# Optimization experiments

Hardware: AMD Instinct MI355X
Metric: run time of the kernel (lower is better)

The kernel has to match this reference:

```python
import jax, jax.numpy as jnp
import numpy as np

B, L, C, R = 2, 1024, 64, 32
RV, DQK, H, NSINK = 32, 64, 8, 4


def setup_inputs() -> dict:
    key = jax.random.key(0)
    ks = jax.random.split(key, 10)
    s_in = 1.0 / np.sqrt(C * R)
    s_r = 1.0 / np.sqrt(R)
    s_rv = 1.0 / np.sqrt(RV)
    return {
        "x": jax.random.normal(ks[0], (B, L, C, R), jnp.float32),
        "Wq": jax.random.normal(ks[1], (C * R, H * DQK), jnp.float32) * s_in,
        "bq": jax.random.normal(ks[2], (H * DQK,), jnp.float32) * s_in,
        "Wk": jax.random.normal(ks[3], (C * R, DQK), jnp.float32) * s_in,
        "bk": jax.random.normal(ks[4], (DQK,), jnp.float32) * s_in,
        "Wv": jax.random.normal(ks[5], (C, R, RV), jnp.float32) * s_r,
        "bv": jax.random.normal(ks[6], (C, RV), jnp.float32) * s_r,
        "Wo": jax.random.normal(ks[7], (C, RV, R), jnp.float32) * s_rv,
        "bo": jax.random.normal(ks[8], (C, R), jnp.float32) * s_rv,
        "sink_q": jax.random.normal(ks[9], (H, NSINK, DQK), jnp.float32),
    }


def reference(x, Wq, bq, Wk, bk, Wv, bv, Wo, bo, sink_q):
    b, l, c, r = x.shape
    h, d_qk = H, DQK
    scale = 1.0 / np.sqrt(d_qk)

    x_flat = x.reshape(b, l, c * r)
    q = (x_flat @ Wq + bq).reshape(b, l, h, d_qk)          # (B,L,H,D)
    k = x_flat @ Wk + bk                                    # (B,L,D) shared MQA key

    # fp32 softmax over time, as in the original
    logits = (jnp.einsum('blhd,bsd->bhls', q, k).astype(jnp.float32) * scale)
    attn = jax.nn.softmax(logits, axis=-1).astype(x.dtype)  # (B,H,L,S)

    # per-channel value projection (B,L,C,RV)
    v = jnp.einsum('blcr,cro->blco', x, Wv) + bv

    # AV with extra channel axis, fused with head-mean (same math as
    # einsum('bhls,bscv->bhlcv').mean(1))
    y = jnp.einsum('bhls,bscv->blcv', attn, v) / h          # (B,L,C,RV)

    # sink-query branch: learned queries attend over time, mean over (H, S)
    logits_s = (jnp.einsum('hsd,bld->bhsl', sink_q, k).astype(jnp.float32) * scale)
    attn_s = jax.nn.softmax(logits_s, axis=-1).astype(x.dtype)  # (B,H,S,L)
    y_sink = jnp.einsum('bhsl,blcv->bcv', attn_s, v) / (h * NSINK)
    y = y + y_sink[:, None]                                 # broadcast over L

    # per-channel output projection + residual
    y = jnp.einsum('blcv,cvr->blcr', y, Wo) + bo
    return x + y
```

## Files before the change

### kernel.cpp

```cpp
#include <hip/hip_runtime.h>
#include <hip/hip_bf16.h>
#include <math.h>


typedef __attribute__((ext_vector_type(8))) short short8;
typedef __attribute__((ext_vector_type(4))) short short4v;
typedef __attribute__((ext_vector_type(4))) float float4v;

__device__ __forceinline__ short f2b(float f) {
    __hip_bfloat16 h = __float2bfloat16(f);
    return __builtin_bit_cast(short, h);
}
__device__ __forceinline__ float b2f(short s) {
    unsigned u = ((unsigned)(unsigned short)s) << 16;
    return __builtin_bit_cast(float, u);
}

__global__ __launch_bounds__(256) void convert_x_kernel(
    const float* __restrict__ src, short* __restrict__ dst, int n4)
{
    int id = blockIdx.x * 256 + threadIdx.x;
    if (id >= n4) return;
    float4 v = reinterpret_cast<const float4*>(src)[id];
    short4v o;
    o[0] = f2b(v.x); o[1] = f2b(v.y); o[2] = f2b(v.z); o[3] = f2b(v.w);
    reinterpret_cast<short4v*>(dst)[id] = o;
}

__global__ __launch_bounds__(256) void convert_w_kernel(
    const float* __restrict__ Wq, const float* __restrict__ Wk,
    short* __restrict__ Wt)
{
    const int n0 = blockIdx.x * 64;
    const int k0 = blockIdx.y * 64;
    const int tid = threadIdx.x;
    __shared__ float ts[64][65];
    for (int i = tid; i < 4096; i += 256) {
        int kk = i >> 6, nn = i & 63;
        int n = n0 + nn, k = k0 + kk;
        float v = (n < 512) ? Wq[(long)k * 512 + n] : Wk[(long)k * 64 + (n - 512)];
        ts[kk][nn] = v;
    }
    __syncthreads();
    for (int i = tid; i < 4096; i += 256) {
        int nn = i >> 6, kk = i & 63;
        Wt[(long)(n0 + nn) * 2048 + k0 + kk] = f2b(ts[kk][nn]);
    }
}

__global__ __launch_bounds__(256) void bias_init_kernel(
    const float* __restrict__ bq, const float* __restrict__ bk,
    float* __restrict__ qk)
{
    const int row = blockIdx.x;
    for (int n = threadIdx.x; n < 576; n += 256)
        qk[(long)row * 576 + n] = (n < 512) ? bq[n] : bk[n - 512];
}

__global__ __launch_bounds__(256) void qkproj_kernel(
    const short* __restrict__ xb, const short* __restrict__ Wt,
    float* __restrict__ qk)
{
    __shared__ short As[64][72];
    __shared__ short Bs[64][72];

    const int tid = threadIdx.x;
    const int wave = tid >> 6;
    const int lane = tid & 63;
    const int wm = wave >> 1, wn = wave & 1;
    const int m15 = lane & 15;
    const int quad = lane >> 4;
    const int row0 = blockIdx.y * 64;
    const int col0 = blockIdx.x * 64;
    const int kbase = blockIdx.z * 1024;

    float4v acc[2][2];
    #pragma unroll
    for (int i = 0; i < 2; ++i)
        #pragma unroll
        for (int j = 0; j < 2; ++j)
            #pragma unroll
            for (int r = 0; r < 4; ++r) acc[i][j][r] = 0.f;

    for (int kt = 0; kt < 16; ++kt) {
        int k0 = kbase + kt * 64;
        #pragma unroll
        for (int p = 0; p < 2; ++p) {
            int i = tid + p * 256;
            int m = i >> 3, kq = i & 7;
            *reinterpret_cast<short8*>(&As[m][kq * 8]) =
                *reinterpret_cast<const short8*>(&xb[(long)(row0 + m) * 2048 + k0 + kq * 8]);
        }
        #pragma unroll
        for (int p = 0; p < 2; ++p) {
            int i = tid + p * 256;
            int n = i >> 3, kq = i & 7;
            *reinterpret_cast<short8*>(&Bs[n][kq * 8]) =
                *reinterpret_cast<const short8*>(&Wt[(long)(col0 + n) * 2048 + k0 + kq * 8]);
        }
        __syncthreads();
        #pragma unroll
        for (int ks = 0; ks < 2; ++ks) {
            short8 a[2], b[2];
            #pragma unroll
            for (int t = 0; t < 2; ++t) {
                a[t] = *reinterpret_cast<const short8*>(&As[wm * 32 + t * 16 + m15][ks * 32 + quad * 8]);
                b[t] = *reinterpret_cast<const short8*>(&Bs[wn * 32 + t * 16 + m15][ks * 32 + quad * 8]);
            }
            #pragma unroll
            for (int ti = 0; ti < 2; ++ti)
                #pragma unroll
                for (int tj = 0; tj < 2; ++tj)
                    acc[ti][tj] = __builtin_amdgcn_mfma_f32_16x16x32_bf16(
                        a[ti], b[tj], acc[ti][tj], 0, 0, 0);
        }
        __syncthreads();
    }

    #pragma unroll
    for (int ti = 0; ti < 2; ++ti)
        #pragma unroll
        for (int r = 0; r < 4; ++r) {
            int row = row0 + wm * 32 + ti * 16 + quad * 4 + r;
            #pragma unroll
            for (int tj = 0; tj < 2; ++tj) {
                int col = col0 + wn * 32 + tj * 16 + m15;
                atomicAdd(&qk[(long)row * 576 + col], acc[ti][tj][r]);
            }
        }
}

__global__ __launch_bounds__(256) void convert_qk_kernel(
    const float* __restrict__ qk, short* __restrict__ qkb)
{
    int id = blockIdx.x * 256 + threadIdx.x;
    float4 v = reinterpret_cast<const float4*>(qk)[id];
    short4v o;
    o[0] = f2b(v.x); o[1] = f2b(v.y); o[2] = f2b(v.z); o[3] = f2b(v.w);
    reinterpret_cast<short4v*>(qkb)[id] = o;
}

__global__ __launch_bounds__(256) void qk_s_kernel(
    const short* __restrict__ qkb, short* __restrict__ S)
{
    const int s0 = blockIdx.x * 64;
    const int l0 = blockIdx.y * 64;
    const int b = blockIdx.z;
    const int tid = threadIdx.x;
    short* Sz = S + ((long)b << 23);

    __shared__ short Qs[64][520];
    __shared__ short Ks[64][72];

    #pragma unroll
    for (int p = 0; p < 16; ++p) {
        int i = tid + p * 256;
        int row = i >> 6, d8 = i & 63;
        *reinterpret_cast<short8*>(&Qs[row][d8 * 8]) =
            *reinterpret_cast<const short8*>(&qkb[(long)((b << 10) + l0 + row) * 576 + d8 * 8]);
    }
    #pragma unroll
    for (int p = 0; p < 2; ++p) {
        int i = tid + p * 256;
        int row = i >> 3, d8 = i & 7;
        *reinterpret_cast<short8*>(&Ks[row][d8 * 8]) =
            *reinterpret_cast<const short8*>(&qkb[(long)((b << 10) + s0 + row) * 576 + 512 + d8 * 8]);
    }
    __syncthreads();

    const int wave = tid >> 6;
    const int lane = tid & 63;
    const int wm = wave >> 1, wn = wave & 1;
    const int m15 = lane & 15;
    const int quad = lane >> 4;

    for (int h = 0; h < 8; ++h) {
        float4v acc[2][2];
        #pragma unroll
        for (int i = 0; i < 2; ++i)
            #pragma unroll
            for (int j = 0; j < 2; ++j)
                #pragma unroll
                for (int r = 0; r < 4; ++r) acc[i][j][r] = 0.f;

        #pragma unroll
        for (int ks = 0; ks < 2; ++ks) {
            short8 a[2], bfr[2];
            #pragma unroll
            for (int t = 0; t < 2; ++t) {
                a[t]   = *reinterpret_cast<const short8*>(
                    &Qs[wm * 32 + t * 16 + m15][h * 64 + ks * 32 + quad * 8]);
                bfr[t] = *reinterpret_cast<const short8*>(
                    &Ks[wn * 32 + t * 16 + m15][ks * 32 + quad * 8]);
            }
            #pragma unroll
            for (int ti = 0; ti < 2; ++ti)
                #pragma unroll
                for (int tj = 0; tj < 2; ++tj)
                    acc[ti][tj] = __builtin_amdgcn_mfma_f32_16x16x32_bf16(
                        a[ti], bfr[tj], acc[ti][tj], 0, 0, 0);
        }

        #pragma unroll
        for (int ti = 0; ti < 2; ++ti)
            #pragma unroll
            for (int r = 0; r < 4; ++r) {
                int l = l0 + wm * 32 + ti * 16 + quad * 4 + r;
                #pragma unroll
                for (int tj = 0; tj < 2; ++tj) {
                    int s = s0 + wn * 32 + tj * 16 + m15;
                    Sz[((long)h << 20) + (l << 10) + s] = f2b(acc[ti][tj][r] * 0.125f);
                }
            }
    }
}

__global__ __launch_bounds__(256) void softmax_avg_kernel(
    const short* __restrict__ S, short* __restrict__ P)
{
    const int l = blockIdx.x;
    const int b = blockIdx.y;
    const int tid = threadIdx.x;
    const int h = tid >> 5, j = tid & 31;
    const short* Sz = S + ((long)b << 23);

    __shared__ float es[8][1032];
    __shared__ float invd[8];

    const short* row = &Sz[((long)h << 20) + (l << 10)];
    float vals[32];
    float pm = -1e30f;
    #pragma unroll
    for (int i = 0; i < 32; ++i) {
        float f = b2f(row[i * 32 + j]);
        vals[i] = f;
        pm = fmaxf(pm, f);
    }
    #pragma unroll
    for (int off = 16; off > 0; off >>= 1) pm = fmaxf(pm, __shfl_down(pm, off, 32));
    pm = __shfl(pm, 0, 32);

    float ps = 0.f;
    #pragma unroll
    for (int i = 0; i < 32; ++i) {
        float e = __expf(vals[i] - pm);
        vals[i] = e;
        ps += e;
    }
    #pragma unroll
    for (int off = 16; off > 0; off >>= 1) ps += __shfl_down(ps, off, 32);
    if (j == 0) invd[h] = 1.f / (8.f * ps);
    __syncthreads();

    const float w = invd[h];
    #pragma unroll
    for (int i = 0; i < 32; ++i) es[h][i * 32 + j] = vals[i] * w;
    __syncthreads();

    for (int s = tid; s < 1024; s += 256) {
        float p = 0.f;
        #pragma unroll
        for (int hh = 0; hh < 8; ++hh) p += es[hh][s];
        P[((long)b << 20) + (l << 10) + s] = f2b(p);
    }
}

__global__ __launch_bounds__(256) void vproj_kernel(
    const float* __restrict__ x, const float* __restrict__ Wv,
    const float* __restrict__ bv, short* __restrict__ vt)
{
    const int c = blockIdx.x;
    const int chunk = blockIdx.y;
    const int b = chunk >> 4;
    const int l0 = (chunk & 15) * 64;
    const int tid = threadIdx.x;
    __shared__ float Wc[32][33];
    __shared__ float xs[64][33];
    for (int i = tid; i < 1024; i += 256)
        Wc[i >> 5][i & 31] = Wv[(c * 32 + (i >> 5)) * 32 + (i & 31)];
    for (int i = tid; i < 2048; i += 256) {
        int s = i >> 5, r = i & 31;
        xs[s][r] = x[((long)(b << 10) + l0 + s) * 2048 + c * 32 + r];
    }
    __syncthreads();
    const int s = tid & 63;
    const int og = tid >> 6;
    #pragma unroll
    for (int oi = 0; oi < 8; ++oi) {
        int o = og * 8 + oi;
        float acc = bv[c * 32 + o];
        #pragma unroll
        for (int r = 0; r < 32; ++r) acc += xs[s][r] * Wc[r][o];
        vt[(long)b * (2048 * 1024) + (long)(c * 32 + o) * 1024 + l0 + s] = f2b(acc);
    }
}

__global__ __launch_bounds__(256) void sink_kernel(
    const float* __restrict__ sink_q, const short* __restrict__ qkb,
    float* __restrict__ Psink)
{
    const int z = blockIdx.x;
    const int b = z >> 5;
    const int idx = z & 31;
    const int tid = threadIdx.x;

    __shared__ float sq[64];
    __shared__ float lgl[1024];
    __shared__ float red[4];
    __shared__ float mxs, invs;

    if (tid < 64) sq[tid] = sink_q[idx * 64 + tid];
    __syncthreads();

    float lmax = -1e30f;
    for (int l = tid; l < 1024; l += 256) {
        const short* kp = &qkb[(long)((b << 10) + l) * 576 + 512];
        float acc = 0.f;
        #pragma unroll
        for (int d8 = 0; d8 < 8; ++d8) {
            short8 kv = *reinterpret_cast<const short8*>(&kp[d8 * 8]);
            #pragma unroll
            for (int j = 0; j < 8; ++j) acc += b2f(kv[j]) * sq[d8 * 8 + j];
        }
        acc *= 0.125f;
        lgl[l] = acc;
        lmax = fmaxf(lmax, acc);
    }
    #pragma unroll
    for (int off = 32; off > 0; off >>= 1) lmax = fmaxf(lmax, __shfl_down(lmax, off, 64));
    if ((tid & 63) == 0) red[tid >> 6] = lmax;
    __syncthreads();
    if (tid == 0) mxs = fmaxf(fmaxf(red[0], red[1]), fmaxf(red[2], red[3]));
    __syncthreads();

    const float m = mxs;
    float psum = 0.f;
    for (int l = tid; l < 1024; l += 256) {
        float e = __expf(lgl[l] - m);
        lgl[l] = e;
        psum += e;
    }
    #pragma unroll
    for (int off = 32; off > 0; off >>= 1) psum += __shfl_down(psum, off, 64);
    if ((tid & 63) == 0) red[tid >> 6] = psum;
    __syncthreads();
    if (tid == 0) invs = 1.f / (red[0] + red[1] + red[2] + red[3]);
    __syncthreads();

    const float wgt = invs * (1.f / 32.f);
    for (int l = tid; l < 1024; l += 256)
        atomicAdd(&Psink[(b << 10) + l], lgl[l] * wgt);
}

__global__ __launch_bounds__(256) void sinky_kernel(
    const float* __restrict__ Psink, const short* __restrict__ vt,
    float* __restrict__ Ysink)
{
    const int b = blockIdx.y;
    const int tid = threadIdx.x;
    __shared__ float ps[1024];
    {
        float4 v = reinterpret_cast<const float4*>(&Psink[b << 10])[tid];
        *reinterpret_cast<float4*>(&ps[tid * 4]) = v;
    }
    __syncthreads();
    const int wave = tid >> 6;
    const int lane = tid & 63;
    const int co = blockIdx.x * 4 + wave;
    const short* vp = &vt[((long)b * 2048 + co) * 1024];
    float acc = 0.f;
    #pragma unroll
    for (int t = 0; t < 16; ++t) {
        int l = t * 64 + lane;
        acc += ps[l] * b2f(vp[l]);
    }
    #pragma unroll
    for (int off = 32; off > 0; off >>= 1) acc += __shfl_down(acc, off, 64);
    if (lane == 0) Ysink[(b << 11) + co] = acc;
}

__global__ __launch_bounds__(256) void y_fused_kernel(
    const short* __restrict__ P, const short* __restrict__ vt,
    const float* __restrict__ Ysink, const float* __restrict__ Wo,
    const float* __restrict__ bo, const float* __restrict__ x,
    float* __restrict__ out)
{
    __shared__ short As[64][72];
    __shared__ short Bs[64][72];

    const int tid = threadIdx.x;
    const int b = blockIdx.z;
    const int col0 = blockIdx.x * 64;
    const int row0 = blockIdx.y * 64;
    const short* Pz = P + ((long)b << 20);
    const short* Vz = vt + ((long)b * 2048 * 1024);

    const int wave = tid >> 6;
    const int lane = tid & 63;
    const int wm = wave >> 1, wn = wave & 1;
    const int m15 = lane & 15;
    const int quad = lane >> 4;

    float4v acc[2][2];
    #pragma unroll
    for (int i = 0; i < 2; ++i)
        #pragma unroll
        for (int j = 0; j < 2; ++j)
            #pragma unroll
            for (int r = 0; r < 4; ++r) acc[i][j][r] = 0.f;

    for (int kt = 0; kt < 16; ++kt) {
        int k0 = kt * 64;
        #pragma unroll
        for (int p = 0; p < 2; ++p) {
            int i = tid + p * 256;
            int m = i >> 3, kq = i & 7;
            *reinterpret_cast<short8*>(&As[m][kq * 8]) =
                *reinterpret_cast<const short8*>(&Pz[(long)(row0 + m) * 1024 + k0 + kq * 8]);
        }
        #pragma unroll
        for (int p = 0; p < 2; ++p) {
            int i = tid + p * 256;
            int n = i >> 3, kq = i & 7;
            *reinterpret_cast<short8*>(&Bs[n][kq * 8]) =
                *reinterpret_cast<const short8*>(&Vz[(long)(col0 + n) * 1024 + k0 + kq * 8]);
        }
        __syncthreads();
        #pragma unroll
        for (int ks = 0; ks < 2; ++ks) {
            short8 a[2], bb[2];
            #pragma unroll
            for (int t = 0; t < 2; ++t) {
                a[t]  = *reinterpret_cast<const short8*>(&As[wm * 32 + t * 16 + m15][ks * 32 + quad * 8]);
                bb[t] = *reinterpret_cast<const short8*>(&Bs[wn * 32 + t * 16 + m15][ks * 32 + quad * 8]);
            }
            #pragma unroll
            for (int ti = 0; ti < 2; ++ti)
                #pragma unroll
                for (int tj = 0; tj < 2; ++tj)
                    acc[ti][tj] = __builtin_amdgcn_mfma_f32_16x16x32_bf16(
                        a[ti], bb[tj], acc[ti][tj], 0, 0, 0);
        }
        __syncthreads();
    }

    float ysv[2];
    #pragma unroll
    for (int tj = 0; tj < 2; ++tj)
        ysv[tj] = Ysink[(b << 11) + col0 + wn * 32 + tj * 16 + m15];

    #pragma unroll
    for (int ti = 0; ti < 2; ++ti)
        #pragma unroll
        for (int r = 0; r < 4; ++r) {
            int row = wm * 32 + ti * 16 + quad * 4 + r;
            #pragma unroll
            for (int tj = 0; tj < 2; ++tj) {
                int col = wn * 32 + tj * 16 + m15;
                As[row][col] = f2b(acc[ti][tj][r] + ysv[tj]);
            }
        }
    const int c0 = col0 >> 5;
    for (int i = tid; i < 4096; i += 256) {
        int n = i >> 6, k = i & 63;
        short v = 0;
        if ((n >> 5) == (k >> 5))
            v = f2b(Wo[((long)(c0 + (n >> 5)) * 32 + (k & 31)) * 32 + (n & 31)]);
        Bs[n][k] = v;
    }
    __syncthreads();

    float4v acc2[2][2];
    #pragma unroll
    for (int i = 0; i < 2; ++i)
        #pragma unroll
        for (int j = 0; j < 2; ++j)
            #pragma unroll
            for (int r = 0; r < 4; ++r) acc2[i][j][r] = 0.f;

    #pragma unroll
    for (int ks = 0; ks < 2; ++ks) {
        short8 a[2], bb[2];
        #pragma unroll
        for (int t = 0; t < 2; ++t) {
            a[t]  = *reinterpret_cast<const short8*>(&As[wm * 32 + t * 16 + m15][ks * 32 + quad * 8]);
            bb[t] = *reinterpret_cast<const short8*>(&Bs[wn * 32 + t * 16 + m15][ks * 32 + quad * 8]);
        }
        #pragma unroll
        for (int ti = 0; ti < 2; ++ti)
            #pragma unroll
            for (int tj = 0; tj < 2; ++tj)
                acc2[ti][tj] = __builtin_amdgcn_mfma_f32_16x16x32_bf16(
                    a[ti], bb[tj], acc2[ti][tj], 0, 0, 0);
    }

    float bov[2];
    #pragma unroll
    for (int tj = 0; tj < 2; ++tj)
        bov[tj] = bo[col0 + wn * 32 + tj * 16 + m15];

    #pragma unroll
    for (int ti = 0; ti < 2; ++ti)
        #pragma unroll
        for (int r = 0; r < 4; ++r) {
            int row = (b << 10) + row0 + wm * 32 + ti * 16 + quad * 4 + r;
            #pragma unroll
            for (int tj = 0; tj < 2; ++tj) {
                int col = col0 + wn * 32 + tj * 16 + m15;
                long oi = (long)row * 2048 + col;
                out[oi] = x[oi] + bov[tj] + acc2[ti][tj][r];
            }
        }
}

extern "C" void kernel_launch(void* const* d_in, const int* in_sizes, int n_in,
                              void* d_out, int out_size, void* d_ws, size_t ws_size,
                              hipStream_t stream)
{
    const float* x  = (const float*)d_in[0];
    const float* Wq = (const float*)d_in[1];
    const float* bq = (const float*)d_in[2];
    const float* Wk = (const float*)d_in[3];
    const float* bk = (const float*)d_in[4];
    const float* Wv = (const float*)d_in[5];
    const float* bv = (const float*)d_in[6];
    const float* Wo = (const float*)d_in[7];
    const float* bo = (const float*)d_in[8];
    const float* sq = (const float*)d_in[9];
    float* out = (float*)d_out;

    float* ws = (float*)d_ws;
    float* qk     = ws;
    short* qkb    = (short*)(ws + 1179648);
    short* P      = (short*)(ws + 1769472);
    float* Psink  = ws + 2818048;
    short* vt     = (short*)(ws + 2820096);
    float* Ysink  = ws + 4917248;
    float* region = ws + 4921344;
    short* xb     = (short*)region;
    short* Wt     = (short*)(region + 2097152);
    short* Sb     = (short*)region;

    dim3 blk(256);

    convert_x_kernel<<<dim3(1024 * 1024 / 256), blk, 0, stream>>>(x, xb, 1048576);
    convert_w_kernel<<<dim3(9, 32), blk, 0, stream>>>(Wq, Wk, Wt);
    bias_init_kernel<<<dim3(2048), blk, 0, stream>>>(bq, bk, qk);
    qkproj_kernel<<<dim3(9, 32, 2), blk, 0, stream>>>(xb, Wt, qk);
    convert_qk_kernel<<<dim3(1152), blk, 0, stream>>>(qk, qkb);
    vproj_kernel<<<dim3(64, 32), blk, 0, stream>>>(x, Wv, bv, vt);
    qk_s_kernel<<<dim3(16, 16, 2), blk, 0, stream>>>(qkb, Sb);
    softmax_avg_kernel<<<dim3(1024, 2), blk, 0, stream>>>(Sb, P);
    hipMemsetAsync(Psink, 0, 2048 * sizeof(float), stream);
    sink_kernel<<<dim3(64), blk, 0, stream>>>(sq, qkb, Psink);
    sinky_kernel<<<dim3(512, 2), blk, 0, stream>>>(Psink, vt, Ysink);
    y_fused_kernel<<<dim3(32, 16, 2), blk, 0, stream>>>(
        P, vt, Ysink, Wo, bo, x, out);
}
```

Measured before the change: 207.7 us.

## Fuse x conversion into vproj, replace split-K atomics with partial buffers, enlarge y tile

The bf16 conversion of x now happens inside the value-projection kernel, which already reads x, so the separate conversion pass and its extra read of x are gone. The split-K QK projection writes two partial buffers with plain stores instead of atomics into a bias-initialised buffer. The bf16 convert kernel then sums the two partials and adds the bias, which removes the bias-init kernel and the atomic traffic. The fused AV/output-projection kernel moves to 128-row tiles, halving the grid and reusing each loaded V tile across more rows, at the cost of more registers and shared memory per block.

```diff
diff --git a/kernel.cpp b/kernel.cpp
--- a/kernel.cpp
+++ b/kernel.cpp
@@ -14,17 +14,6 @@
 __device__ __forceinline__ float b2f(short s) {
     unsigned u = ((unsigned)(unsigned short)s) << 16;
     return __builtin_bit_cast(float, u);
-}
-
-__global__ __launch_bounds__(256) void convert_x_kernel(
-    const float* __restrict__ src, short* __restrict__ dst, int n4)
-{
-    int id = blockIdx.x * 256 + threadIdx.x;
-    if (id >= n4) return;
-    float4 v = reinterpret_cast<const float4*>(src)[id];
-    short4v o;
-    o[0] = f2b(v.x); o[1] = f2b(v.y); o[2] = f2b(v.z); o[3] = f2b(v.w);
-    reinterpret_cast<short4v*>(dst)[id] = o;
 }
 
 __global__ __launch_bounds__(256) void convert_w_kernel(
@@ -48,18 +37,43 @@
     }
 }
 
-__global__ __launch_bounds__(256) void bias_init_kernel(
-    const float* __restrict__ bq, const float* __restrict__ bk,
-    float* __restrict__ qk)
-{
-    const int row = blockIdx.x;
-    for (int n = threadIdx.x; n < 576; n += 256)
-        qk[(long)row * 576 + n] = (n < 512) ? bq[n] : bk[n - 512];
+__global__ __launch_bounds__(256) void vproj_kernel(
+    const float* __restrict__ x, const float* __restrict__ Wv,
+    const float* __restrict__ bv, short* __restrict__ vt,
+    short* __restrict__ xb)
+{
+    const int c = blockIdx.x;
+    const int chunk = blockIdx.y;
+    const int b = chunk >> 4;
+    const int l0 = (chunk & 15) * 64;
+    const int tid = threadIdx.x;
+    __shared__ float Wc[32][33];
+    __shared__ float xs[64][33];
+    for (int i = tid; i < 1024; i += 256)
+        Wc[i >> 5][i & 31] = Wv[(c * 32 + (i >> 5)) * 32 + (i & 31)];
+    for (int i = tid; i < 2048; i += 256) {
+        int s = i >> 5, r = i & 31;
+        long gi = ((long)(b << 10) + l0 + s) * 2048 + c * 32 + r;
+        float v = x[gi];
+        xs[s][r] = v;
+        xb[gi] = f2b(v);
+    }
+    __syncthreads();
+    const int s = tid & 63;
+    const int og = tid >> 6;
+    #pragma unroll
+    for (int oi = 0; oi < 8; ++oi) {
+        int o = og * 8 + oi;
+        float acc = bv[c * 32 + o];
+        #pragma unroll
+        for (int r = 0; r < 32; ++r) acc += xs[s][r] * Wc[r][o];
+        vt[(long)b * (2048 * 1024) + (long)(c * 32 + o) * 1024 + l0 + s] = f2b(acc);
+    }
 }
 
 __global__ __launch_bounds__(256) void qkproj_kernel(
     const short* __restrict__ xb, const short* __restrict__ Wt,
-    float* __restrict__ qk)
+    float* __restrict__ qkpart)
 {
     __shared__ short As[64][72];
     __shared__ short Bs[64][72];
@@ -73,6 +87,7 @@
     const int row0 = blockIdx.y * 64;
     const int col0 = blockIdx.x * 64;
     const int kbase = blockIdx.z * 1024;
+    float* outz = qkpart + (long)blockIdx.z * 1179648;
 
     float4v acc[2][2];
     #pragma unroll
@@ -125,18 +140,27 @@
             #pragma unroll
             for (int tj = 0; tj < 2; ++tj) {
                 int col = col0 + wn * 32 + tj * 16 + m15;
-                atomicAdd(&qk[(long)row * 576 + col], acc[ti][tj][r]);
+                outz[(long)row * 576 + col] = acc[ti][tj][r];
             }
         }
 }
 
 __global__ __launch_bounds__(256) void convert_qk_kernel(
-    const float* __restrict__ qk, short* __restrict__ qkb)
+    const float* __restrict__ qkpart, const float* __restrict__ bq,
+    const float* __restrict__ bk, short* __restrict__ qkb)
 {
     int id = blockIdx.x * 256 + threadIdx.x;
-    float4 v = reinterpret_cast<const float4*>(qk)[id];
+    float4 a = reinterpret_cast<const float4*>(qkpart)[id];
+    float4 b = reinterpret_cast<const float4*>(qkpart + 1179648)[id];
+    int col4 = (id % 144) * 4;
+    float4 bias = (col4 < 512)
+        ? *reinterpret_cast<const float4*>(&bq[col4])
+        : *reinterpret_cast<const float4*>(&bk[col4 - 512]);
     short4v o;
-    o[0] = f2b(v.x); o[1] = f2b(v.y); o[2] = f2b(v.z); o[3] = f2b(v.w);
+    o[0] = f2b(a.x + b.x + bias.x);
+    o[1] = f2b(a.y + b.y + bias.y);
+    o[2] = f2b(a.z + b.z + bias.z);
+    o[3] = f2b(a.w + b.w + bias.w);
     reinterpret_cast<short4v*>(qkb)[id] = o;
 }
 
@@ -265,36 +289,6 @@
     }
 }
 
-__global__ __launch_bounds__(256) void vproj_kernel(
-    const float* __restrict__ x, const float* __restrict__ Wv,
-    const float* __restrict__ bv, short* __restrict__ vt)
-{
-    const int c = blockIdx.x;
-    const int chunk = blockIdx.y;
-    const int b = chunk >> 4;
-    const int l0 = (chunk & 15) * 64;
-    const int tid = threadIdx.x;
-    __shared__ float Wc[32][33];
-    __shared__ float xs[64][33];
-    for (int i = tid; i < 1024; i += 256)
-        Wc[i >> 5][i & 31] = Wv[(c * 32 + (i >> 5)) * 32 + (i & 31)];
-    for (int i = tid; i < 2048; i += 256) {
-        int s = i >> 5, r = i & 31;
-        xs[s][r] = x[((long)(b << 10) + l0 + s) * 2048 + c * 32 + r];
-    }
-    __syncthreads();
-    const int s = tid & 63;
-    const int og = tid >> 6;
-    #pragma unroll
-    for (int oi = 0; oi < 8; ++oi) {
-        int o = og * 8 + oi;
-        float acc = bv[c * 32 + o];
-        #pragma unroll
-        for (int r = 0; r < 32; ++r) acc += xs[s][r] * Wc[r][o];
-        vt[(long)b * (2048 * 1024) + (long)(c * 32 + o) * 1024 + l0 + s] = f2b(acc);
-    }
-}
-
 __global__ __launch_bounds__(256) void sink_kernel(
     const float* __restrict__ sink_q, const short* __restrict__ qkb,
     float* __restrict__ Psink)
@@ -385,13 +379,13 @@
     const float* __restrict__ bo, const float* __restrict__ x,
     float* __restrict__ out)
 {
-    __shared__ short As[64][72];
+    __shared__ short As[128][72];
     __shared__ short Bs[64][72];
 
     const int tid = threadIdx.x;
     const int b = blockIdx.z;
     const int col0 = blockIdx.x * 64;
-    const int row0 = blockIdx.y * 64;
+    const int row0 = blockIdx.y * 128;
     const short* Pz = P + ((long)b << 20);
     const short* Vz = vt + ((long)b * 2048 * 1024);
 
@@ -401,9 +395,9 @@
     const int m15 = lane & 15;
     const int quad = lane >> 4;
 
-    float4v acc[2][2];
-    #pragma unroll
-    for (int i = 0; i < 2; ++i)
+    float4v acc[4][2];
+    #pragma unroll
+    for (int i = 0; i < 4; ++i)
         #pragma unroll
         for (int j = 0; j < 2; ++j)
             #pragma unroll
@@ -412,7 +406,7 @@
     for (int kt = 0; kt < 16; ++kt) {
         int k0 = kt * 64;
         #pragma unroll
-        for (int p = 0; p < 2; ++p) {
+        for (int p = 0; p < 4; ++p) {
             int i = tid + p * 256;
             int m = i >> 3, kq = i & 7;
             *reinterpret_cast<short8*>(&As[m][kq * 8]) =
@@ -428,14 +422,15 @@
         __syncthreads();
         #pragma unroll
         for (int ks = 0; ks < 2; ++ks) {
-            short8 a[2], bb[2];
-            #pragma unroll
-            for (int t = 0; t < 2; ++t) {
-                a[t]  = *reinterpret_cast<const short8*>(&As[wm * 32 + t * 16 + m15][ks * 32 + quad * 8]);
+            short8 a[4], bb[2];
+            #pragma unroll
+            for (int t = 0; t < 4; ++t)
+                a[t] = *reinterpret_cast<const short8*>(&As[wm * 64 + t * 16 + m15][ks * 32 + quad * 8]);
+            #pragma unroll
+            for (int t = 0; t < 2; ++t)
                 bb[t] = *reinterpret_cast<const short8*>(&Bs[wn * 32 + t * 16 + m15][ks * 32 + quad * 8]);
-            }
-            #pragma unroll
-            for (int ti = 0; ti < 2; ++ti)
+            #pragma unroll
+            for (int ti = 0; ti < 4; ++ti)
                 #pragma unroll
                 for (int tj = 0; tj < 2; ++tj)
                     acc[ti][tj] = __builtin_amdgcn_mfma_f32_16x16x32_bf16(
@@ -450,10 +445,10 @@
         ysv[tj] = Ysink[(b << 11) + col0 + wn * 32 + tj * 16 + m15];
 
     #pragma unroll
-    for (int ti = 0; ti < 2; ++ti)
+    for (int ti = 0; ti < 4; ++ti)
         #pragma unroll
         for (int r = 0; r < 4; ++r) {
-            int row = wm * 32 + ti * 16 + quad * 4 + r;
+            int row = wm * 64 + ti * 16 + quad * 4 + r;
             #pragma unroll
             for (int tj = 0; tj < 2; ++tj) {
                 int col = wn * 32 + tj * 16 + m15;
@@ -470,9 +465,9 @@
     }
     __syncthreads();
 
-    float4v acc2[2][2];
-    #pragma unroll
-    for (int i = 0; i < 2; ++i)
+    float4v acc2[4][2];
+    #pragma unroll
+    for (int i = 0; i < 4; ++i)
         #pragma unroll
         for (int j = 0; j < 2; ++j)
             #pragma unroll
@@ -480,14 +475,15 @@
 
     #pragma unroll
     for (int ks = 0; ks < 2; ++ks) {
-        short8 a[2], bb[2];
-        #pragma unroll
-        for (int t = 0; t < 2; ++t) {
-            a[t]  = *reinterpret_cast<const short8*>(&As[wm * 32 + t * 16 + m15][ks * 32 + quad * 8]);
+        short8 a[4], bb[2];
+        #pragma unroll
+        for (int t = 0; t < 4; ++t)
+            a[t] = *reinterpret_cast<const short8*>(&As[wm * 64 + t * 16 + m15][ks * 32 + quad * 8]);
+        #pragma unroll
+        for (int t = 0; t < 2; ++t)
             bb[t] = *reinterpret_cast<const short8*>(&Bs[wn * 32 + t * 16 + m15][ks * 32 + quad * 8]);
-        }
-        #pragma unroll
-        for (int ti = 0; ti < 2; ++ti)
+        #pragma unroll
+        for (int ti = 0; ti < 4; ++ti)
             #pragma unroll
             for (int tj = 0; tj < 2; ++tj)
                 acc2[ti][tj] = __builtin_amdgcn_mfma_f32_16x16x32_bf16(
@@ -500,10 +496,10 @@
         bov[tj] = bo[col0 + wn * 32 + tj * 16 + m15];
 
     #pragma unroll
-    for (int ti = 0; ti < 2; ++ti)
+    for (int ti = 0; ti < 4; ++ti)
         #pragma unroll
         for (int r = 0; r < 4; ++r) {
-            int row = (b << 10) + row0 + wm * 32 + ti * 16 + quad * 4 + r;
+            int row = (b << 10) + row0 + wm * 64 + ti * 16 + quad * 4 + r;
             #pragma unroll
             for (int tj = 0; tj < 2; ++tj) {
                 int col = col0 + wn * 32 + tj * 16 + m15;
@@ -530,30 +526,28 @@
     float* out = (float*)d_out;
 
     float* ws = (float*)d_ws;
-    float* qk     = ws;
-    short* qkb    = (short*)(ws + 1179648);
-    short* P      = (short*)(ws + 1769472);
-    float* Psink  = ws + 2818048;
-    short* vt     = (short*)(ws + 2820096);
-    float* Ysink  = ws + 4917248;
-    float* region = ws + 4921344;
+    float* qkpart = ws;
+    short* qkb    = (short*)(ws + 2359296);
+    short* P      = (short*)(ws + 2949120);
+    float* Psink  = ws + 3997696;
+    short* vt     = (short*)(ws + 3999744);
+    float* Ysink  = ws + 6096896;
+    float* region = ws + 6100992;
     short* xb     = (short*)region;
     short* Wt     = (short*)(region + 2097152);
     short* Sb     = (short*)region;
 
     dim3 blk(256);
 
-    convert_x_kernel<<<dim3(1024 * 1024 / 256), blk, 0, stream>>>(x, xb, 1048576);
     convert_w_kernel<<<dim3(9, 32), blk, 0, stream>>>(Wq, Wk, Wt);
-    bias_init_kernel<<<dim3(2048), blk, 0, stream>>>(bq, bk, qk);
-    qkproj_kernel<<<dim3(9, 32, 2), blk, 0, stream>>>(xb, Wt, qk);
-    convert_qk_kernel<<<dim3(1152), blk, 0, stream>>>(qk, qkb);
-    vproj_kernel<<<dim3(64, 32), blk, 0, stream>>>(x, Wv, bv, vt);
+    vproj_kernel<<<dim3(64, 32), blk, 0, stream>>>(x, Wv, bv, vt, xb);
+    qkproj_kernel<<<dim3(9, 32, 2), blk, 0, stream>>>(xb, Wt, qkpart);
+    convert_qk_kernel<<<dim3(1152), blk, 0, stream>>>(qkpart, bq, bk, qkb);
     qk_s_kernel<<<dim3(16, 16, 2), blk, 0, stream>>>(qkb, Sb);
     softmax_avg_kernel<<<dim3(1024, 2), blk, 0, stream>>>(Sb, P);
     hipMemsetAsync(Psink, 0, 2048 * sizeof(float), stream);
     sink_kernel<<<dim3(64), blk, 0, stream>>>(sq, qkb, Psink);
     sinky_kernel<<<dim3(512, 2), blk, 0, stream>>>(Psink, vt, Ysink);
-    y_fused_kernel<<<dim3(32, 16, 2), blk, 0, stream>>>(
+    y_fused_kernel<<<dim3(32, 8, 2), blk, 0, stream>>>(
         P, vt, Ysink, Wo, bo, x, out);
 }
```

New measurement: 194.2 us. 6.5% less time.
